# Performance work log

Hardware: AMD Instinct MI355X
Metric: run time of the kernel (lower is better)

The kernel has to match this reference:

```python
import jax, jax.numpy as jnp
import numpy as np


def _layernorm(x, g, b):
    # keras LayerNormalization default epsilon = 1e-3
    m = jnp.mean(x, axis=-1, keepdims=True)
    v = jnp.var(x, axis=-1, keepdims=True)
    return (x - m) * jax.lax.rsqrt(v + 1e-3) * g + b


def _gat(x, mask, W, a_src, a_dst, b):
    # PyG-style GATConv with concat heads, expressed densely over the
    # thresholded adjacency mask (edges where adj > 0.5; mask[i, j] = edge j->i).
    # x: [B, N, Din], W: [Din, H, C], mask: [N, N] bool
    h = jnp.einsum('bnd,dhc->bnhc', x, W)                 # [B,N,H,C]
    s_src = jnp.einsum('bnhc,hc->bhn', h, a_src)          # [B,H,N]
    s_dst = jnp.einsum('bnhc,hc->bhn', h, a_dst)          # [B,H,N]
    e = jax.nn.leaky_relu(s_dst[:, :, :, None] + s_src[:, :, None, :], 0.2)  # [B,H,i,j]
    e = jnp.where(mask[None, None], e, jnp.float32(-1e9))
    alpha = jax.nn.softmax(e, axis=-1)                    # softmax over neighbors j
    out = jnp.einsum('bhij,bjhc->bihc', alpha, h)         # aggregate messages
    B, N, H, C = out.shape
    return out.reshape(B, N, H * C) + b


def setup_inputs() -> dict:
    key = jax.random.key(0)
    ks = jax.random.split(key, 20)
    B, T, N, F = 4, 24, 500, 3
    HID, OUT, HEADS = 8, 16, 4      # SpatialProcessor(num_nodes, 3, 8, 16)
    D, AH, KD, FF = 16, 2, 8, 32    # EfficientTransformer(16, heads=2, ff_dim=32)
    n = lambda k, shape, sc=0.3: jax.random.normal(k, shape, dtype=jnp.float32) * sc
    z = lambda shape: jnp.zeros(shape, jnp.float32)
    return {
        'x': jax.random.normal(ks[0], (B, T, N, F), dtype=jnp.float32),
        'embedding': jax.random.normal(ks[1], (N, HID), dtype=jnp.float32),
        'proj_w': n(ks[2], (F, HID)), 'proj_b': z((HID,)),
        'g1_w': n(ks[3], (HID, HEADS, HID // HEADS)),
        'g1_as': n(ks[4], (HEADS, HID // HEADS)),
        'g1_ad': n(ks[5], (HEADS, HID // HEADS)),
        'g1_b': z((HID,)),
        'g2_w': n(ks[6], (HID, HEADS, OUT // HEADS)),
        'g2_as': n(ks[7], (HEADS, OUT // HEADS)),
        'g2_ad': n(ks[8], (HEADS, OUT // HEADS)),
        'g2_b': z((OUT,)),
        'wq': n(ks[9], (D, AH, KD)), 'bq': z((AH, KD)),
        'wk': n(ks[10], (D, AH, KD)), 'bk': z((AH, KD)),
        'wv': n(ks[11], (D, AH, KD)), 'bv': z((AH, KD)),
        'wo': n(ks[12], (AH, KD, D)), 'bo': z((D,)),
        'ln1_g': jnp.ones((D,), jnp.float32), 'ln1_b': z((D,)),
        'ln2_g': jnp.ones((D,), jnp.float32), 'ln2_b': z((D,)),
        'f_w1': n(ks[13], (D, FF)), 'f_b1': z((FF,)),
        'f_w2': n(ks[14], (FF, D)), 'f_b2': z((D,)),
        'r_w1': n(ks[15], (D, D)), 'r_b1': z((D,)),
        'r_w2': n(ks[16], (D, 1)), 'r_b2': z((1,)),
    }


def reference(x, embedding, proj_w, proj_b, g1_w, g1_as, g1_ad, g1_b,
              g2_w, g2_as, g2_ad, g2_b, wq, bq, wk, bk, wv, bv, wo, bo,
              ln1_g, ln1_b, ln2_g, ln2_b, f_w1, f_b1, f_w2, f_b2,
              r_w1, r_b1, r_w2, r_b2):
    B, T, N, F = x.shape
    # AdaptiveAdjacency: cosine similarity of learned node embeddings,
    # identical across batch; edges extracted where adj > 0.5 (diag is 1 -> self loops)
    ne = embedding * jax.lax.rsqrt(jnp.sum(embedding * embedding, -1, keepdims=True))
    adj = ne @ ne.T
    mask = adj > 0.5                                   # [N, N] bool
    # SpatialProcessor over B*T independent graphs
    h = x.reshape(B * T, N, F) @ proj_w + proj_b        # Dense proj -> [BT, N, 8]
    h = jax.nn.gelu(_gat(h, mask, g1_w, g1_as, g1_ad, g1_b), approximate=False)
    h = _gat(h, mask, g2_w, g2_as, g2_ad, g2_b)         # [BT, N, 16]
    D = h.shape[-1]
    # Faithful to original: raw tf.reshape [B,T,N,16] -> [B*N, T, 16] (no transpose)
    t = h.reshape(B * N, T, D)
    # keras MultiHeadAttention(heads=2, key_dim=8), 1 transformer layer
    q = jnp.einsum('bse,ehd->bshd', t, wq) + bq
    k = jnp.einsum('bse,ehd->bshd', t, wk) + bk
    v = jnp.einsum('bse,ehd->bshd', t, wv) + bv
    scale = jnp.sqrt(jnp.asarray(q.shape[-1], jnp.float32))
    att = jax.nn.softmax(jnp.einsum('bshd,bthd->bhst', q, k) / scale, axis=-1)
    o = jnp.einsum('bhst,bthd->bshd', att, v)
    o = jnp.einsum('bshd,hde->bse', o, wo) + bo
    t = _layernorm(t + o, ln1_g, ln1_b)
    ffn = jax.nn.gelu(t @ f_w1 + f_b1, approximate=False) @ f_w2 + f_b2
    t = _layernorm(t + ffn, ln2_g, ln2_b)
    pooled = t.reshape(B, N, T, D).mean(axis=2)
    r = jax.nn.gelu(pooled @ r_w1 + r_b1, approximate=False) @ r_w2 + r_b2
    return r[..., 0]
```

## Files before the change

kernel.cpp:

```cpp
#include <hip/hip_runtime.h>
#include <math.h>
#include <type_traits>

#define DEV __device__ __forceinline__

DEV float gelu_exact(float x) {
    return 0.5f * x * (1.0f + erff(x * 0.70710678118654752f));
}

__global__ __launch_bounds__(512)
void mask_kernel(const float* __restrict__ emb,
                 unsigned short* __restrict__ nbr,
                 int* __restrict__ deg) {
    const int i = blockIdx.x;
    const int j = threadIdx.x;
    float ei[8], ej[8];
    float si = 0.f, sj = 0.f;
#pragma unroll
    for (int e = 0; e < 8; ++e) { ei[e] = emb[i * 8 + e]; si += ei[e] * ei[e]; }
    const int jj = (j < 500) ? j : 0;
#pragma unroll
    for (int e = 0; e < 8; ++e) { ej[e] = emb[jj * 8 + e]; sj += ej[e] * ej[e]; }
    const float ri = 1.0f / sqrtf(si);
    const float rj = 1.0f / sqrtf(sj);
    float dot = 0.f;
#pragma unroll
    for (int e = 0; e < 8; ++e) dot += (ei[e] * ri) * (ej[e] * rj);
    const bool pred = (j < 500) && (dot > 0.5f);
    const unsigned long long m = __ballot(pred);

    __shared__ unsigned wcnt[8];
    const int wave = j >> 6, lane = j & 63;
    if (lane == 0) wcnt[wave] = (unsigned)__popcll(m);
    __syncthreads();
    unsigned off = 0;
    for (int w = 0; w < wave; ++w) off += wcnt[w];
    if (pred) {
        const unsigned pos = off + (unsigned)__popcll(m & ((1ull << lane) - 1ull));
        if (pos < 128) nbr[i * 128 + pos] = (unsigned short)j;
    }
    if (j == 0) {
        unsigned t = 0;
        for (int w = 0; w < 8; ++w) t += wcnt[w];
        deg[i] = (int)(t > 128u ? 128u : t);
    }
}

template <int C, int OUTS, bool PROJ, bool GELU_OUT>
__global__ __launch_bounds__(512)
void gat_kernel(const float* __restrict__ in,
                const float* __restrict__ pw,
                const float* __restrict__ pb,
                const float* __restrict__ W,
                const float* __restrict__ asrc,
                const float* __restrict__ adst,
                const float* __restrict__ bias,
                const unsigned short* __restrict__ nbr,
                const int* __restrict__ deg,
                float* __restrict__ out) {
    using Vec = std::conditional_t<C == 2, float2, float4>;
    const int b = blockIdx.x >> 2;
    const int head = blockIdx.x & 3;
    const int tid = threadIdx.x;
    __shared__ float xh[500 * 9];
    __shared__ Vec h1[500];
    __shared__ float ssrc[500];
    __shared__ float sdst[500];

    if (tid < 500) {
        if constexpr (PROJ) {
            const float* xr = in + ((size_t)b * 500 + tid) * 3;
            const float x0 = xr[0], x1 = xr[1], x2 = xr[2];
#pragma unroll
            for (int e = 0; e < 8; ++e)
                xh[tid * 9 + e] = x0 * pw[e] + x1 * pw[8 + e] + x2 * pw[16 + e] + pb[e];
        } else {
            const float4* xr = (const float4*)(in + ((size_t)b * 500 + tid) * 8);
            const float4 v0 = xr[0], v1 = xr[1];
            xh[tid * 9 + 0] = v0.x; xh[tid * 9 + 1] = v0.y;
            xh[tid * 9 + 2] = v0.z; xh[tid * 9 + 3] = v0.w;
            xh[tid * 9 + 4] = v1.x; xh[tid * 9 + 5] = v1.y;
            xh[tid * 9 + 6] = v1.z; xh[tid * 9 + 7] = v1.w;
        }
    }
    __syncthreads();

    if (tid < 500) {
        float xv[8];
#pragma unroll
        for (int e = 0; e < 8; ++e) xv[e] = xh[tid * 9 + e];
        float acc[C];
#pragma unroll
        for (int c = 0; c < C; ++c) acc[c] = 0.f;
#pragma unroll
        for (int e = 0; e < 8; ++e) {
            const float xe = xv[e];
#pragma unroll
            for (int c = 0; c < C; ++c) acc[c] += xe * W[(e * 4 + head) * C + c];
        }
        float ss = 0.f, sd = 0.f;
#pragma unroll
        for (int c = 0; c < C; ++c) {
            ss += acc[c] * asrc[head * C + c];
            sd += acc[c] * adst[head * C + c];
        }
        Vec hv;
        if constexpr (C == 2) { hv.x = acc[0]; hv.y = acc[1]; }
        else { hv.x = acc[0]; hv.y = acc[1]; hv.z = acc[2]; hv.w = acc[3]; }
        h1[tid] = hv;
        ssrc[tid] = ss;
        sdst[tid] = sd;
    }
    __syncthreads();

    if (tid < 500) {
        const int i = tid;
        const float dd = sdst[i];
        const int dg = deg[i];
        const unsigned short* nb = nbr + i * 128;
        float num[C];
#pragma unroll
        for (int c = 0; c < C; ++c) num[c] = 0.f;
        float den = 0.f;
        int k = 0;
        for (; k + 4 <= dg; k += 4) {
            const ushort4 j4 = *(const ushort4*)(nb + k);
            float e0 = dd + ssrc[j4.x]; e0 = (e0 > 0.f) ? e0 : 0.2f * e0;
            float e1 = dd + ssrc[j4.y]; e1 = (e1 > 0.f) ? e1 : 0.2f * e1;
            float e2 = dd + ssrc[j4.z]; e2 = (e2 > 0.f) ? e2 : 0.2f * e2;
            float e3 = dd + ssrc[j4.w]; e3 = (e3 > 0.f) ? e3 : 0.2f * e3;
            const float w0 = __expf(e0), w1 = __expf(e1);
            const float w2 = __expf(e2), w3 = __expf(e3);
            const Vec ha = h1[j4.x], hb = h1[j4.y], hc = h1[j4.z], hd = h1[j4.w];
            den += (w0 + w1) + (w2 + w3);
            if constexpr (C == 2) {
                num[0] += (w0 * ha.x + w1 * hb.x) + (w2 * hc.x + w3 * hd.x);
                num[1] += (w0 * ha.y + w1 * hb.y) + (w2 * hc.y + w3 * hd.y);
            } else {
                num[0] += (w0 * ha.x + w1 * hb.x) + (w2 * hc.x + w3 * hd.x);
                num[1] += (w0 * ha.y + w1 * hb.y) + (w2 * hc.y + w3 * hd.y);
                num[2] += (w0 * ha.z + w1 * hb.z) + (w2 * hc.z + w3 * hd.z);
                num[3] += (w0 * ha.w + w1 * hb.w) + (w2 * hc.w + w3 * hd.w);
            }
        }
        for (; k < dg; ++k) {
            const int j = nb[k];
            float e = dd + ssrc[j];
            e = (e > 0.f) ? e : 0.2f * e;
            const float w = __expf(e);
            den += w;
            const Vec hj = h1[j];
            if constexpr (C == 2) { num[0] += w * hj.x; num[1] += w * hj.y; }
            else { num[0] += w * hj.x; num[1] += w * hj.y;
                   num[2] += w * hj.z; num[3] += w * hj.w; }
        }
        const float inv = 1.0f / den;
        float* orow = out + ((size_t)b * 500 + i) * OUTS + head * C;
#pragma unroll
        for (int c = 0; c < C; ++c) {
            float v = num[c] * inv + bias[head * C + c];
            if constexpr (GELU_OUT) v = gelu_exact(v);
            orow[c] = v;
        }
    }
}

__global__ __launch_bounds__(64)
void transformer_kernel(const float* __restrict__ tin,
                        const float* __restrict__ wq, const float* __restrict__ bq,
                        const float* __restrict__ wk, const float* __restrict__ bk,
                        const float* __restrict__ wv, const float* __restrict__ bv,
                        const float* __restrict__ wo, const float* __restrict__ bo,
                        const float* __restrict__ ln1g, const float* __restrict__ ln1b,
                        const float* __restrict__ ln2g, const float* __restrict__ ln2b,
                        const float* __restrict__ fw1, const float* __restrict__ fb1,
                        const float* __restrict__ fw2, const float* __restrict__ fb2,
                        const float* __restrict__ rw1, const float* __restrict__ rb1,
                        const float* __restrict__ rw2, const float* __restrict__ rb2,
                        float* __restrict__ outp) {
    const int r = blockIdx.x;
    const int lane = threadIdx.x;
    const int d = lane & 15;
    const int srow = lane >> 4;
    const int f = lane & 31;
    const int s2 = lane >> 5;
    __shared__ float t0[24][16], qs[24][16], ks[24][16], vs[24][16];
    __shared__ float os[24][16], t1[24][16], hid[24][32], pooled[16];

    const float4* row4 = (const float4*)(tin + (size_t)r * 384);
    float4* t04 = (float4*)&t0[0][0];
#pragma unroll 1
    for (int idx = lane; idx < 96; idx += 64) t04[idx] = row4[idx];
    float wqc[16], wkc[16], wvc[16];
#pragma unroll
    for (int e = 0; e < 16; ++e) {
        wqc[e] = wq[e * 16 + d];
        wkc[e] = wk[e * 16 + d];
        wvc[e] = wv[e * 16 + d];
    }
    const float bqv = bq[d], bkv = bk[d], bvv = bv[d];
    __syncthreads();

#pragma unroll 1
    for (int it = 0; it < 6; ++it) {
        const int s = it * 4 + srow;
        const float4 r0 = *(const float4*)&t0[s][0];
        const float4 r1 = *(const float4*)&t0[s][4];
        const float4 r2 = *(const float4*)&t0[s][8];
        const float4 r3 = *(const float4*)&t0[s][12];
        const float te[16] = {r0.x, r0.y, r0.z, r0.w, r1.x, r1.y, r1.z, r1.w,
                              r2.x, r2.y, r2.z, r2.w, r3.x, r3.y, r3.z, r3.w};
        float aq = bqv, ak = bkv, av = bvv;
#pragma unroll
        for (int e = 0; e < 16; ++e) {
            aq += te[e] * wqc[e];
            ak += te[e] * wkc[e];
            av += te[e] * wvc[e];
        }
        qs[s][d] = aq; ks[s][d] = ak; vs[s][d] = av;
    }
    __syncthreads();

    if (lane < 48) {
        const int h = lane / 24, s = lane % 24;
        const float4 q0 = *(const float4*)&qs[s][h * 8];
        const float4 q1 = *(const float4*)&qs[s][h * 8 + 4];
        float sc[24];
        float mx = -1e30f;
#pragma unroll
        for (int t = 0; t < 24; ++t) {
            const float4 k0 = *(const float4*)&ks[t][h * 8];
            const float4 k1 = *(const float4*)&ks[t][h * 8 + 4];
            float a = q0.x * k0.x + q0.y * k0.y + q0.z * k0.z + q0.w * k0.w +
                      q1.x * k1.x + q1.y * k1.y + q1.z * k1.z + q1.w * k1.w;
            a *= 0.35355339059327373f;
            sc[t] = a;
            mx = fmaxf(mx, a);
        }
        float sum = 0.f;
#pragma unroll
        for (int t = 0; t < 24; ++t) { sc[t] = __expf(sc[t] - mx); sum += sc[t]; }
        const float inv = 1.0f / sum;
        float o0x = 0.f, o0y = 0.f, o0z = 0.f, o0w = 0.f;
        float o1x = 0.f, o1y = 0.f, o1z = 0.f, o1w = 0.f;
#pragma unroll
        for (int t = 0; t < 24; ++t) {
            const float4 v0 = *(const float4*)&vs[t][h * 8];
            const float4 v1 = *(const float4*)&vs[t][h * 8 + 4];
            const float w = sc[t];
            o0x += w * v0.x; o0y += w * v0.y; o0z += w * v0.z; o0w += w * v0.w;
            o1x += w * v1.x; o1y += w * v1.y; o1z += w * v1.z; o1w += w * v1.w;
        }
        float4 ov0 = {o0x * inv, o0y * inv, o0z * inv, o0w * inv};
        float4 ov1 = {o1x * inv, o1y * inv, o1z * inv, o1w * inv};
        *(float4*)&os[s][h * 8] = ov0;
        *(float4*)&os[s][h * 8 + 4] = ov1;
    }
    float woc[16];
#pragma unroll
    for (int hd = 0; hd < 16; ++hd) woc[hd] = wo[hd * 16 + d];
    const float bov = bo[d];
    const float g1v = ln1g[d], be1v = ln1b[d];
    __syncthreads();

#pragma unroll 1
    for (int it = 0; it < 6; ++it) {
        const int s = it * 4 + srow;
        const float4 r0 = *(const float4*)&os[s][0];
        const float4 r1 = *(const float4*)&os[s][4];
        const float4 r2 = *(const float4*)&os[s][8];
        const float4 r3 = *(const float4*)&os[s][12];
        const float oe[16] = {r0.x, r0.y, r0.z, r0.w, r1.x, r1.y, r1.z, r1.w,
                              r2.x, r2.y, r2.z, r2.w, r3.x, r3.y, r3.z, r3.w};
        float a = bov;
#pragma unroll
        for (int hd = 0; hd < 16; ++hd) a += oe[hd] * woc[hd];
        const float xv = t0[s][d] + a;
        float s1 = xv, sq = xv * xv;
        s1 += __shfl_xor(s1, 1); sq += __shfl_xor(sq, 1);
        s1 += __shfl_xor(s1, 2); sq += __shfl_xor(sq, 2);
        s1 += __shfl_xor(s1, 4); sq += __shfl_xor(sq, 4);
        s1 += __shfl_xor(s1, 8); sq += __shfl_xor(sq, 8);
        const float mean = s1 * 0.0625f;
        const float var = fmaxf(sq * 0.0625f - mean * mean, 0.f);
        t1[s][d] = (xv - mean) * rsqrtf(var + 1e-3f) * g1v + be1v;
    }
    float f1c[16];
#pragma unroll
    for (int e = 0; e < 16; ++e) f1c[e] = fw1[e * 32 + f];
    const float fb1v = fb1[f];
    __syncthreads();

#pragma unroll 1
    for (int it = 0; it < 12; ++it) {
        const int s = it * 2 + s2;
        const float4 r0 = *(const float4*)&t1[s][0];
        const float4 r1 = *(const float4*)&t1[s][4];
        const float4 r2 = *(const float4*)&t1[s][8];
        const float4 r3 = *(const float4*)&t1[s][12];
        const float te[16] = {r0.x, r0.y, r0.z, r0.w, r1.x, r1.y, r1.z, r1.w,
                              r2.x, r2.y, r2.z, r2.w, r3.x, r3.y, r3.z, r3.w};
        float a = fb1v;
#pragma unroll
        for (int e = 0; e < 16; ++e) a += te[e] * f1c[e];
        hid[s][f] = gelu_exact(a);
    }
    float f2c[32];
#pragma unroll
    for (int ff = 0; ff < 32; ++ff) f2c[ff] = fw2[ff * 16 + d];
    const float fb2v = fb2[d];
    const float g2v = ln2g[d], be2v = ln2b[d];
    __syncthreads();

    float pacc = 0.f;
#pragma unroll 1
    for (int it = 0; it < 6; ++it) {
        const int s = it * 4 + srow;
        float he[32];
#pragma unroll
        for (int q8 = 0; q8 < 8; ++q8) {
            const float4 rv = *(const float4*)&hid[s][q8 * 4];
            he[q8 * 4 + 0] = rv.x; he[q8 * 4 + 1] = rv.y;
            he[q8 * 4 + 2] = rv.z; he[q8 * 4 + 3] = rv.w;
        }
        float a = fb2v;
#pragma unroll
        for (int ff = 0; ff < 32; ++ff) a += he[ff] * f2c[ff];
        const float xv = t1[s][d] + a;
        float s1 = xv, sq = xv * xv;
        s1 += __shfl_xor(s1, 1); sq += __shfl_xor(sq, 1);
        s1 += __shfl_xor(s1, 2); sq += __shfl_xor(sq, 2);
        s1 += __shfl_xor(s1, 4); sq += __shfl_xor(sq, 4);
        s1 += __shfl_xor(s1, 8); sq += __shfl_xor(sq, 8);
        const float mean = s1 * 0.0625f;
        const float var = fmaxf(sq * 0.0625f - mean * mean, 0.f);
        pacc += (xv - mean) * rsqrtf(var + 1e-3f) * g2v + be2v;
    }
    pacc += __shfl_xor(pacc, 16);
    pacc += __shfl_xor(pacc, 32);
    if (lane < 16) pooled[lane] = pacc * (1.0f / 24.0f);
    __syncthreads();

    float partial = 0.f;
    if (lane < 16) {
        float a = rb1[lane];
#pragma unroll
        for (int e = 0; e < 16; ++e) a += pooled[e] * rw1[e * 16 + lane];
        partial = gelu_exact(a) * rw2[lane];
    }
    partial += __shfl_xor(partial, 8);
    partial += __shfl_xor(partial, 4);
    partial += __shfl_xor(partial, 2);
    partial += __shfl_xor(partial, 1);
    if (lane == 0) outp[r] = partial + rb2[0];
}

extern "C" void kernel_launch(void* const* d_in, const int* in_sizes, int n_in,
                              void* d_out, int out_size, void* d_ws, size_t ws_size,
                              hipStream_t stream) {
    const float* x      = (const float*)d_in[0];
    const float* emb    = (const float*)d_in[1];
    const float* proj_w = (const float*)d_in[2];
    const float* proj_b = (const float*)d_in[3];
    const float* g1_w   = (const float*)d_in[4];
    const float* g1_as  = (const float*)d_in[5];
    const float* g1_ad  = (const float*)d_in[6];
    const float* g1_b   = (const float*)d_in[7];
    const float* g2_w   = (const float*)d_in[8];
    const float* g2_as  = (const float*)d_in[9];
    const float* g2_ad  = (const float*)d_in[10];
    const float* g2_b   = (const float*)d_in[11];
    const float* wq = (const float*)d_in[12];
    const float* bq = (const float*)d_in[13];
    const float* wk = (const float*)d_in[14];
    const float* bk = (const float*)d_in[15];
    const float* wv = (const float*)d_in[16];
    const float* bv = (const float*)d_in[17];
    const float* wo = (const float*)d_in[18];
    const float* bo = (const float*)d_in[19];
    const float* ln1g = (const float*)d_in[20];
    const float* ln1b = (const float*)d_in[21];
    const float* ln2g = (const float*)d_in[22];
    const float* ln2b = (const float*)d_in[23];
    const float* fw1 = (const float*)d_in[24];
    const float* fb1 = (const float*)d_in[25];
    const float* fw2 = (const float*)d_in[26];
    const float* fb2 = (const float*)d_in[27];
    const float* rw1 = (const float*)d_in[28];
    const float* rb1 = (const float*)d_in[29];
    const float* rw2 = (const float*)d_in[30];
    const float* rb2 = (const float*)d_in[31];

    unsigned short* nbr = (unsigned short*)d_ws;
    int* deg   = (int*)((char*)d_ws + 131072);
    float* h_g1  = (float*)((char*)d_ws + 135168);
    float* t_buf = (float*)((char*)d_ws + 135168 + 1536000);

    mask_kernel<<<500, 512, 0, stream>>>(emb, nbr, deg);
    gat_kernel<2, 8, true, true><<<384, 512, 0, stream>>>(
        x, proj_w, proj_b, g1_w, g1_as, g1_ad, g1_b, nbr, deg, h_g1);
    gat_kernel<4, 16, false, false><<<384, 512, 0, stream>>>(
        h_g1, nullptr, nullptr, g2_w, g2_as, g2_ad, g2_b, nbr, deg, t_buf);
    transformer_kernel<<<2000, 64, 0, stream>>>(
        t_buf, wq, bq, wk, bk, wv, bv, wo, bo, ln1g, ln1b, ln2g, ln2b,
        fw1, fb1, fw2, fb2, rw1, rb1, rw2, rb2, (float*)d_out);
}
```

Before: 50.47 us.

## Repartition GAT work: all heads per block, node slices, split neighbor lists across thread pairs

Each GAT block now computes the projected features for all four heads of one graph, then handles a 63-node slice across all heads. Each node-head's neighbor list is split between two lanes whose partial sums are combined with a shuffle. The grid doubles, and the per-thread serial aggregation loop is shorter, which cuts latency from imbalanced degrees. In exchange, the 4-head projection is redundantly recomputed 8 times per graph, and strided shared-memory gathers may cause more bank conflicts.

```diff
diff --git a/kernel.cpp b/kernel.cpp
--- a/kernel.cpp
+++ b/kernel.cpp
@@ -59,79 +59,86 @@
                 const int* __restrict__ deg,
                 float* __restrict__ out) {
     using Vec = std::conditional_t<C == 2, float2, float4>;
-    const int b = blockIdx.x >> 2;
-    const int head = blockIdx.x & 3;
+    constexpr int HSTR = (C == 2) ? 10 : 20;
+    const int b = blockIdx.x >> 3;
+    const int slice = blockIdx.x & 7;
     const int tid = threadIdx.x;
-    __shared__ float xh[500 * 9];
-    __shared__ Vec h1[500];
-    __shared__ float ssrc[500];
-    __shared__ float sdst[500];
+    __shared__ float h1[500 * HSTR];
+    __shared__ float ssrc[4 * 516];
 
     if (tid < 500) {
+        float xv[8];
         if constexpr (PROJ) {
             const float* xr = in + ((size_t)b * 500 + tid) * 3;
             const float x0 = xr[0], x1 = xr[1], x2 = xr[2];
 #pragma unroll
             for (int e = 0; e < 8; ++e)
-                xh[tid * 9 + e] = x0 * pw[e] + x1 * pw[8 + e] + x2 * pw[16 + e] + pb[e];
+                xv[e] = x0 * pw[e] + x1 * pw[8 + e] + x2 * pw[16 + e] + pb[e];
         } else {
             const float4* xr = (const float4*)(in + ((size_t)b * 500 + tid) * 8);
             const float4 v0 = xr[0], v1 = xr[1];
-            xh[tid * 9 + 0] = v0.x; xh[tid * 9 + 1] = v0.y;
-            xh[tid * 9 + 2] = v0.z; xh[tid * 9 + 3] = v0.w;
-            xh[tid * 9 + 4] = v1.x; xh[tid * 9 + 5] = v1.y;
-            xh[tid * 9 + 6] = v1.z; xh[tid * 9 + 7] = v1.w;
-        }
-    }
-    __syncthreads();
-
-    if (tid < 500) {
-        float xv[8];
-#pragma unroll
-        for (int e = 0; e < 8; ++e) xv[e] = xh[tid * 9 + e];
-        float acc[C];
-#pragma unroll
-        for (int c = 0; c < C; ++c) acc[c] = 0.f;
-#pragma unroll
-        for (int e = 0; e < 8; ++e) {
-            const float xe = xv[e];
-#pragma unroll
-            for (int c = 0; c < C; ++c) acc[c] += xe * W[(e * 4 + head) * C + c];
-        }
-        float ss = 0.f, sd = 0.f;
-#pragma unroll
-        for (int c = 0; c < C; ++c) {
-            ss += acc[c] * asrc[head * C + c];
-            sd += acc[c] * adst[head * C + c];
-        }
-        Vec hv;
-        if constexpr (C == 2) { hv.x = acc[0]; hv.y = acc[1]; }
-        else { hv.x = acc[0]; hv.y = acc[1]; hv.z = acc[2]; hv.w = acc[3]; }
-        h1[tid] = hv;
-        ssrc[tid] = ss;
-        sdst[tid] = sd;
-    }
-    __syncthreads();
-
-    if (tid < 500) {
-        const int i = tid;
-        const float dd = sdst[i];
+            xv[0] = v0.x; xv[1] = v0.y; xv[2] = v0.z; xv[3] = v0.w;
+            xv[4] = v1.x; xv[5] = v1.y; xv[6] = v1.z; xv[7] = v1.w;
+        }
+#pragma unroll
+        for (int h = 0; h < 4; ++h) {
+            float acc[C];
+#pragma unroll
+            for (int c = 0; c < C; ++c) acc[c] = 0.f;
+#pragma unroll
+            for (int e = 0; e < 8; ++e) {
+                const float xe = xv[e];
+#pragma unroll
+                for (int c = 0; c < C; ++c) acc[c] += xe * W[(e * 4 + h) * C + c];
+            }
+            float ss = 0.f;
+            Vec hv;
+#pragma unroll
+            for (int c = 0; c < C; ++c) ss += acc[c] * asrc[h * C + c];
+            if constexpr (C == 2) { hv.x = acc[0]; hv.y = acc[1]; }
+            else { hv.x = acc[0]; hv.y = acc[1]; hv.z = acc[2]; hv.w = acc[3]; }
+            *(Vec*)&h1[tid * HSTR + h * C] = hv;
+            ssrc[h * 516 + tid] = ss;
+        }
+    }
+    __syncthreads();
+
+    const int pairId = tid >> 1;
+    const int half = tid & 1;
+    const int h = pairId & 3;
+    const int local = pairId >> 2;
+    const int i = slice * 63 + local;
+    const bool valid = (local < 63) && (i < 500);
+    float num[C];
+#pragma unroll
+    for (int c = 0; c < C; ++c) num[c] = 0.f;
+    float den = 0.f;
+    if (valid) {
+        float dd = 0.f;
+        {
+            const Vec hi = *(const Vec*)&h1[i * HSTR + h * C];
+            if constexpr (C == 2) dd = hi.x * adst[h * 2] + hi.y * adst[h * 2 + 1];
+            else dd = hi.x * adst[h * 4] + hi.y * adst[h * 4 + 1] +
+                      hi.z * adst[h * 4 + 2] + hi.w * adst[h * 4 + 3];
+        }
         const int dg = deg[i];
+        const int k0 = half ? (dg >> 1) : 0;
+        const int k1 = half ? dg : (dg >> 1);
         const unsigned short* nb = nbr + i * 128;
-        float num[C];
-#pragma unroll
-        for (int c = 0; c < C; ++c) num[c] = 0.f;
-        float den = 0.f;
-        int k = 0;
-        for (; k + 4 <= dg; k += 4) {
-            const ushort4 j4 = *(const ushort4*)(nb + k);
-            float e0 = dd + ssrc[j4.x]; e0 = (e0 > 0.f) ? e0 : 0.2f * e0;
-            float e1 = dd + ssrc[j4.y]; e1 = (e1 > 0.f) ? e1 : 0.2f * e1;
-            float e2 = dd + ssrc[j4.z]; e2 = (e2 > 0.f) ? e2 : 0.2f * e2;
-            float e3 = dd + ssrc[j4.w]; e3 = (e3 > 0.f) ? e3 : 0.2f * e3;
+        const float* sr = ssrc + h * 516;
+        int k = k0;
+        for (; k + 4 <= k1; k += 4) {
+            const int j0 = nb[k], j1 = nb[k + 1], j2 = nb[k + 2], j3 = nb[k + 3];
+            float e0 = dd + sr[j0]; e0 = (e0 > 0.f) ? e0 : 0.2f * e0;
+            float e1 = dd + sr[j1]; e1 = (e1 > 0.f) ? e1 : 0.2f * e1;
+            float e2 = dd + sr[j2]; e2 = (e2 > 0.f) ? e2 : 0.2f * e2;
+            float e3 = dd + sr[j3]; e3 = (e3 > 0.f) ? e3 : 0.2f * e3;
             const float w0 = __expf(e0), w1 = __expf(e1);
             const float w2 = __expf(e2), w3 = __expf(e3);
-            const Vec ha = h1[j4.x], hb = h1[j4.y], hc = h1[j4.z], hd = h1[j4.w];
+            const Vec ha = *(const Vec*)&h1[j0 * HSTR + h * C];
+            const Vec hb = *(const Vec*)&h1[j1 * HSTR + h * C];
+            const Vec hc = *(const Vec*)&h1[j2 * HSTR + h * C];
+            const Vec hd = *(const Vec*)&h1[j3 * HSTR + h * C];
             den += (w0 + w1) + (w2 + w3);
             if constexpr (C == 2) {
                 num[0] += (w0 * ha.x + w1 * hb.x) + (w2 * hc.x + w3 * hd.x);
@@ -143,22 +150,27 @@
                 num[3] += (w0 * ha.w + w1 * hb.w) + (w2 * hc.w + w3 * hd.w);
             }
         }
-        for (; k < dg; ++k) {
+        for (; k < k1; ++k) {
             const int j = nb[k];
-            float e = dd + ssrc[j];
+            float e = dd + sr[j];
             e = (e > 0.f) ? e : 0.2f * e;
             const float w = __expf(e);
             den += w;
-            const Vec hj = h1[j];
+            const Vec hj = *(const Vec*)&h1[j * HSTR + h * C];
             if constexpr (C == 2) { num[0] += w * hj.x; num[1] += w * hj.y; }
             else { num[0] += w * hj.x; num[1] += w * hj.y;
                    num[2] += w * hj.z; num[3] += w * hj.w; }
         }
+    }
+    den += __shfl_xor(den, 1);
+#pragma unroll
+    for (int c = 0; c < C; ++c) num[c] += __shfl_xor(num[c], 1);
+    if (valid && half == 0) {
         const float inv = 1.0f / den;
-        float* orow = out + ((size_t)b * 500 + i) * OUTS + head * C;
+        float* orow = out + ((size_t)b * 500 + i) * OUTS + h * C;
 #pragma unroll
         for (int c = 0; c < C; ++c) {
-            float v = num[c] * inv + bias[head * C + c];
+            float v = num[c] * inv + bias[h * C + c];
             if constexpr (GELU_OUT) v = gelu_exact(v);
             orow[c] = v;
         }
@@ -397,9 +409,9 @@
     float* t_buf = (float*)((char*)d_ws + 135168 + 1536000);
 
     mask_kernel<<<500, 512, 0, stream>>>(emb, nbr, deg);
-    gat_kernel<2, 8, true, true><<<384, 512, 0, stream>>>(
+    gat_kernel<2, 8, true, true><<<768, 512, 0, stream>>>(
         x, proj_w, proj_b, g1_w, g1_as, g1_ad, g1_b, nbr, deg, h_g1);
-    gat_kernel<4, 16, false, false><<<384, 512, 0, stream>>>(
+    gat_kernel<4, 16, false, false><<<768, 512, 0, stream>>>(
         h_g1, nullptr, nullptr, g2_w, g2_as, g2_ad, g2_b, nbr, deg, t_buf);
     transformer_kernel<<<2000, 64, 0, stream>>>(
         t_buf, wq, bq, wk, bk, wv, bv, wo, bo, ln1g, ln1b, ln2g, ln2b,
```

Measured after the change: 43.70 us. 13.4% less time.
